# Optimization experiments

Measured on AMD Instinct MI355X. Metric: run time of the kernel, lower is better.

The kernel has to match this reference:

```python
import jax, jax.numpy as jnp
import numpy as np

B, Dx, Dz, Dy, H = 4096, 512, 512, 256, 2048
T0, T1 = 0.0, 1.0
N_STEPS = 64


def setup_inputs() -> dict:
    key = jax.random.key(0)
    ks = jax.random.split(key, 9)
    X = jax.random.normal(ks[0], (B, Dx), jnp.float32)
    # P sampled Uniform(0.01, 0.1) as in the torch module
    P = jax.random.uniform(ks[1], (Dz, Dx), jnp.float32, 0.01, 0.1)
    # A scaled so spectral radius ~1 -> exp(A*T) stays bounded over the integration
    A = jax.random.normal(ks[2], (Dz, Dz), jnp.float32) * (Dz ** -0.5)
    W1 = jax.random.normal(ks[3], (H, Dz), jnp.float32) * (Dz ** -0.5)
    b1 = jax.random.normal(ks[4], (H,), jnp.float32) * 0.01
    W2 = jax.random.normal(ks[5], (H, H), jnp.float32) * (H ** -0.5)
    b2 = jax.random.normal(ks[6], (H,), jnp.float32) * 0.01
    W3 = jax.random.normal(ks[7], (Dy, H), jnp.float32) * (H ** -0.5)
    b3 = jax.random.normal(ks[8], (Dy,), jnp.float32) * 0.01
    return dict(X=X, P=P, A=A, W1=W1, b1=b1, W2=W2, b2=b2, W3=W3, b3=b3,
                n_steps=N_STEPS)


def reference(X, P, A, W1, b1, W2, b2, W3, b3, n_steps):
    # Z0 = einsum('ji,bi->bj', P, X)  -> projection into latent ODE state
    z0 = X @ P.T  # [B, Dz]
    dt = jnp.float32((T1 - T0) / n_steps)

    def f(z):  # dz/dt = A z, batched: einsum('ji,bi->bj', A, z)
        return z @ A.T

    def rk4_step(z, _):
        k1 = f(z)
        k2 = f(z + 0.5 * dt * k1)
        k3 = f(z + 0.5 * dt * k2)
        k4 = f(z + dt * k3)
        return z + (dt / 6.0) * (k1 + 2.0 * k2 + 2.0 * k3 + k4), None

    zT, _ = jax.lax.scan(rk4_step, z0, None, length=n_steps)  # [B, Dz]

    # QnnMatrixODE MLP head (n_layers=3): Lin+ReLU, Lin+ReLU, Lin
    h = jax.nn.relu(zT @ W1.T + b1)
    h = jax.nn.relu(h @ W2.T + b2)
    y = h @ W3.T + b3  # [B, Dy]
    return y
```

## Files before the change

kernel.cpp:

```cpp
#include <hip/hip_runtime.h>

#define BDIM 4096
#define DX 512
#define DZ 512
#define DY 256
#define HD 2048
#define NSTEPS 64
#define LDT 72

typedef __attribute__((ext_vector_type(8))) short bf16x8;
typedef __attribute__((ext_vector_type(4))) float f32x4;

__device__ inline unsigned short f2bf(float f) {
    unsigned u = __float_as_uint(f);
    unsigned r = 0x7FFFu + ((u >> 16) & 1u);
    return (unsigned short)((u + r) >> 16);
}
__device__ inline float bf2f(unsigned short h) {
    return __uint_as_float(((unsigned)h) << 16);
}

#define GLDS16(g, l)                                                            \
    __builtin_amdgcn_global_load_lds((const __attribute__((address_space(1))) void*)(g), \
                                     (__attribute__((address_space(3))) void*)(l), 16, 0, 0)

struct CvtJobs {
    const float* src[5];
    unsigned short* hi[5];
    unsigned short* lo[5];
    int n4[5];
};
__global__ __launch_bounds__(256) void cvt_multi_k(CvtJobs J) {
    const int j = blockIdx.y;
    const int i4 = blockIdx.x * 256 + threadIdx.x;
    if (i4 >= J.n4[j]) return;
    float4 v = ((const float4*)J.src[j])[i4];
    ushort4 h;
    h.x = f2bf(v.x); h.y = f2bf(v.y); h.z = f2bf(v.z); h.w = f2bf(v.w);
    ((ushort4*)J.hi[j])[i4] = h;
    if (J.lo[j]) {
        ushort4 l;
        l.x = f2bf(v.x - bf2f(h.x));
        l.y = f2bf(v.y - bf2f(h.y));
        l.z = f2bf(v.z - bf2f(h.z));
        l.w = f2bf(v.w - bf2f(h.w));
        ((ushort4*)J.lo[j])[i4] = l;
    }
}

__global__ __launch_bounds__(256) void split_t_k(const float* __restrict__ A0,
                                                 unsigned short* __restrict__ H0,
                                                 unsigned short* __restrict__ L0,
                                                 const float* __restrict__ A1,
                                                 unsigned short* __restrict__ H1,
                                                 unsigned short* __restrict__ L1, int D) {
    const float* A = blockIdx.z ? A1 : A0;
    unsigned short* HT = blockIdx.z ? H1 : H0;
    unsigned short* LT = blockIdx.z ? L1 : L0;
    __shared__ float t[32][33];
    const int bx = blockIdx.x * 32, by = blockIdx.y * 32;
    const int x = threadIdx.x, y = threadIdx.y;
#pragma unroll
    for (int dy = 0; dy < 32; dy += 8)
        t[y + dy][x] = A[(size_t)(by + y + dy) * D + bx + x];
    __syncthreads();
#pragma unroll
    for (int dy = 0; dy < 32; dy += 8) {
        float v = t[x][y + dy];
        unsigned short h = f2bf(v);
        size_t o = (size_t)(bx + y + dy) * D + by + x;
        HT[o] = h;
        LT[o] = f2bf(v - bf2f(h));
    }
}

__global__ __launch_bounds__(256) void taylor_t_k(const float* __restrict__ Am,
                                                  const float* __restrict__ M2f,
                                                  const float* __restrict__ M3f,
                                                  const float* __restrict__ M4f,
                                                  unsigned short* __restrict__ Sh,
                                                  unsigned short* __restrict__ Sl,
                                                  unsigned short* __restrict__ STh,
                                                  unsigned short* __restrict__ STl,
                                                  int D, float h) {
    __shared__ float t[32][33];
    const float c2 = 0.5f * h * h;
    const float c3 = h * h * h * (1.0f / 6.0f);
    const float c4 = h * h * h * h * (1.0f / 24.0f);
    const int bx = blockIdx.x * 32, by = blockIdx.y * 32;
    const int x = threadIdx.x, y = threadIdx.y;
#pragma unroll
    for (int dy = 0; dy < 32; dy += 8) {
        const int row = by + y + dy, col = bx + x;
        const size_t idx = (size_t)row * D + col;
        float s = h * Am[idx] + c2 * M2f[idx] + c3 * M3f[idx] + c4 * M4f[idx];
        if (row == col) s += 1.0f;
        t[y + dy][x] = s;
        unsigned short hi = f2bf(s);
        Sh[idx] = hi;
        Sl[idx] = f2bf(s - bf2f(hi));
    }
    __syncthreads();
#pragma unroll
    for (int dy = 0; dy < 32; dy += 8) {
        float s = t[x][y + dy];
        size_t o = (size_t)(bx + y + dy) * D + by + x;
        unsigned short hi = f2bf(s);
        STh[o] = hi;
        STl[o] = f2bf(s - bf2f(hi));
    }
}

struct G64In { const unsigned short *Ahi, *Alo, *Bhi, *Blo; };
struct G64Out { float* Cf32; unsigned short *Chi, *Clo, *CThi, *CTlo; };

__device__ __forceinline__ void g64_core(int bx, int by, int M, int N, int K,
                                         G64In in, G64Out o,
                                         unsigned short* Ash, unsigned short* Asl,
                                         unsigned short* Bsh, unsigned short* Bsl) {
    const int tid = threadIdx.x;
    const int lane = tid & 63;
    const int wave = tid >> 6;
    const int wr = wave >> 1, wc = wave & 1;
    const int row0 = by * 64, col0 = bx * 64;
    const int sr = tid >> 2;
    const int sk = (tid & 3) * 16;

    const int niter = K >> 6;
    bf16x8 pa0, pa1, pl0, pl1, pb0, pb1, pq0, pq1;
    {
        const unsigned short* ar = in.Ahi + (size_t)(row0 + sr) * K + sk;
        const unsigned short* al = in.Alo + (size_t)(row0 + sr) * K + sk;
        const unsigned short* br = in.Bhi + (size_t)(col0 + sr) * K + sk;
        const unsigned short* bl = in.Blo + (size_t)(col0 + sr) * K + sk;
        pa0 = *(const bf16x8*)ar; pa1 = *(const bf16x8*)(ar + 8);
        pl0 = *(const bf16x8*)al; pl1 = *(const bf16x8*)(al + 8);
        pb0 = *(const bf16x8*)br; pb1 = *(const bf16x8*)(br + 8);
        pq0 = *(const bf16x8*)bl; pq1 = *(const bf16x8*)(bl + 8);
    }

    f32x4 acc[4] = {};
    const int mb = wr * 32 + (lane & 15);
    const int nb = wc * 32 + (lane & 15);

    for (int it = 0; it < niter; ++it) {
        __syncthreads();
        *(bf16x8*)&Ash[sr * LDT + sk] = pa0; *(bf16x8*)&Ash[sr * LDT + sk + 8] = pa1;
        *(bf16x8*)&Asl[sr * LDT + sk] = pl0; *(bf16x8*)&Asl[sr * LDT + sk + 8] = pl1;
        *(bf16x8*)&Bsh[sr * LDT + sk] = pb0; *(bf16x8*)&Bsh[sr * LDT + sk + 8] = pb1;
        *(bf16x8*)&Bsl[sr * LDT + sk] = pq0; *(bf16x8*)&Bsl[sr * LDT + sk + 8] = pq1;
        __syncthreads();

        {
            const int kn = (it + 1 < niter) ? ((it + 1) << 6) : 0;
            const unsigned short* ar = in.Ahi + (size_t)(row0 + sr) * K + kn + sk;
            const unsigned short* al = in.Alo + (size_t)(row0 + sr) * K + kn + sk;
            const unsigned short* br = in.Bhi + (size_t)(col0 + sr) * K + kn + sk;
            const unsigned short* bl = in.Blo + (size_t)(col0 + sr) * K + kn + sk;
            pa0 = *(const bf16x8*)ar; pa1 = *(const bf16x8*)(ar + 8);
            pl0 = *(const bf16x8*)al; pl1 = *(const bf16x8*)(al + 8);
            pb0 = *(const bf16x8*)br; pb1 = *(const bf16x8*)(br + 8);
            pq0 = *(const bf16x8*)bl; pq1 = *(const bf16x8*)(bl + 8);
        }

#pragma unroll
        for (int kh = 0; kh < 2; ++kh) {
            const int kk = kh * 32 + (lane >> 4) * 8;
            bf16x8 ah[2], alx[2], bh[2], blx[2];
#pragma unroll
            for (int t = 0; t < 2; ++t) {
                ah[t]  = *(const bf16x8*)&Ash[(mb + t * 16) * LDT + kk];
                alx[t] = *(const bf16x8*)&Asl[(mb + t * 16) * LDT + kk];
                bh[t]  = *(const bf16x8*)&Bsh[(nb + t * 16) * LDT + kk];
                blx[t] = *(const bf16x8*)&Bsl[(nb + t * 16) * LDT + kk];
            }
#pragma unroll
            for (int mt = 0; mt < 2; ++mt)
#pragma unroll
                for (int nt = 0; nt < 2; ++nt) {
                    acc[mt * 2 + nt] = __builtin_amdgcn_mfma_f32_16x16x32_bf16(
                        ah[mt], bh[nt], acc[mt * 2 + nt], 0, 0, 0);
                    acc[mt * 2 + nt] = __builtin_amdgcn_mfma_f32_16x16x32_bf16(
                        ah[mt], blx[nt], acc[mt * 2 + nt], 0, 0, 0);
                    acc[mt * 2 + nt] = __builtin_amdgcn_mfma_f32_16x16x32_bf16(
                        alx[mt], bh[nt], acc[mt * 2 + nt], 0, 0, 0);
                }
        }
    }

#pragma unroll
    for (int mt = 0; mt < 2; ++mt) {
        const int grow = row0 + wr * 32 + mt * 16 + (lane >> 4) * 4;
#pragma unroll
        for (int nt = 0; nt < 2; ++nt) {
            const int gcol = col0 + wc * 32 + nt * 16 + (lane & 15);
            f32x4 a = acc[mt * 2 + nt];
            unsigned short h4[4], l4[4];
#pragma unroll
            for (int i = 0; i < 4; ++i) {
                h4[i] = f2bf(a[i]);
                l4[i] = f2bf(a[i] - bf2f(h4[i]));
            }
            if (o.Cf32) {
#pragma unroll
                for (int i = 0; i < 4; ++i) o.Cf32[(size_t)(grow + i) * N + gcol] = a[i];
            }
            if (o.Chi) {
#pragma unroll
                for (int i = 0; i < 4; ++i) o.Chi[(size_t)(grow + i) * N + gcol] = h4[i];
            }
            if (o.Clo) {
#pragma unroll
                for (int i = 0; i < 4; ++i) o.Clo[(size_t)(grow + i) * N + gcol] = l4[i];
            }
            if (o.CThi) {
                ushort4 u = {h4[0], h4[1], h4[2], h4[3]};
                *(ushort4*)&o.CThi[(size_t)gcol * M + grow] = u;
            }
            if (o.CTlo) {
                ushort4 u = {l4[0], l4[1], l4[2], l4[3]};
                *(ushort4*)&o.CTlo[(size_t)gcol * M + grow] = u;
            }
        }
    }
}

__global__ __launch_bounds__(256) void g64_one(G64In in, G64Out o, int M, int N, int K) {
    __shared__ unsigned short Ash[64 * LDT], Asl[64 * LDT], Bsh[64 * LDT], Bsl[64 * LDT];
    g64_core(blockIdx.x, blockIdx.y, M, N, K, in, o, Ash, Asl, Bsh, Bsl);
}

__global__ __launch_bounds__(256) void g64_dual(G64In i0, G64Out o0, G64In i1, G64Out o1,
                                                int M, int N, int K) {
    __shared__ unsigned short Ash[64 * LDT], Asl[64 * LDT], Bsh[64 * LDT], Bsl[64 * LDT];
    g64_core(blockIdx.x, blockIdx.y, M, N, K, blockIdx.z ? i1 : i0, blockIdx.z ? o1 : o0,
             Ash, Asl, Bsh, Bsl);
}

template <int RELU, int BIAS, int OUT_BF16>
__global__ __launch_bounds__(256) void gemm_bf16(int M, int N, int K,
                                                 const unsigned short* __restrict__ A,
                                                 const unsigned short* __restrict__ B,
                                                 void* __restrict__ C,
                                                 const float* __restrict__ bias) {
    __shared__ unsigned short As[128 * 32];
    __shared__ unsigned short Bs[128 * 32];

    const int tid = threadIdx.x;
    const int lane = tid & 63;
    const int wave = tid >> 6;
    const int wr = wave >> 1, wc = wave & 1;
    const int row0 = blockIdx.y * 128;
    const int col0 = blockIdx.x * 128;

    const int srow = lane >> 2;
    const int schunk = (lane & 3) * 8;

    f32x4 acc[4][4] = {};

    for (int k0 = 0; k0 < K; k0 += 32) {
        const int r0 = wave * 32;
        GLDS16(A + (size_t)(row0 + r0 + srow) * K + k0 + schunk, &As[r0 * 32]);
        GLDS16(A + (size_t)(row0 + r0 + 16 + srow) * K + k0 + schunk, &As[(r0 + 16) * 32]);
        GLDS16(B + (size_t)(col0 + r0 + srow) * K + k0 + schunk, &Bs[r0 * 32]);
        GLDS16(B + (size_t)(col0 + r0 + 16 + srow) * K + k0 + schunk, &Bs[(r0 + 16) * 32]);
        __syncthreads();

        const int kk = (lane >> 4) * 8;
        const int mbase = wr * 64 + (lane & 15);
        const int nbase = wc * 64 + (lane & 15);
        bf16x8 af[4], bf[4];
#pragma unroll
        for (int t = 0; t < 4; ++t) {
            af[t] = *(const bf16x8*)&As[(mbase + t * 16) * 32 + kk];
            bf[t] = *(const bf16x8*)&Bs[(nbase + t * 16) * 32 + kk];
        }
#pragma unroll
        for (int mt = 0; mt < 4; ++mt)
#pragma unroll
            for (int nt = 0; nt < 4; ++nt)
                acc[mt][nt] = __builtin_amdgcn_mfma_f32_16x16x32_bf16(af[mt], bf[nt],
                                                                      acc[mt][nt], 0, 0, 0);
        __syncthreads();
    }

#pragma unroll
    for (int mt = 0; mt < 4; ++mt) {
        const int grow = row0 + wr * 64 + mt * 16 + (lane >> 4) * 4;
#pragma unroll
        for (int nt = 0; nt < 4; ++nt) {
            const int gcol = col0 + wc * 64 + nt * 16 + (lane & 15);
            const float bv = BIAS ? bias[gcol] : 0.0f;
#pragma unroll
            for (int i = 0; i < 4; ++i) {
                float v = acc[mt][nt][i] + bv;
                if (RELU) v = fmaxf(v, 0.0f);
                const size_t off = (size_t)(grow + i) * N + gcol;
                if (OUT_BF16)
                    ((unsigned short*)C)[off] = f2bf(v);
                else
                    ((float*)C)[off] = v;
            }
        }
    }
}

__global__ __launch_bounds__(256) void gemm64nt_f32(int M, int N, int K,
                                                    const unsigned short* __restrict__ A,
                                                    const unsigned short* __restrict__ B,
                                                    float* __restrict__ C,
                                                    const float* __restrict__ bias) {
    __shared__ unsigned short As[64 * 32];
    __shared__ unsigned short Bs[64 * 32];
    const int tid = threadIdx.x;
    const int lane = tid & 63;
    const int wave = tid >> 6;
    const int wr = wave >> 1, wc = wave & 1;
    const int row0 = blockIdx.y * 64;
    const int col0 = blockIdx.x * 64;
    const int r = tid >> 2, kq = (tid & 3) * 8;

    f32x4 acc[4] = {};

    for (int k0 = 0; k0 < K; k0 += 32) {
        bf16x8 av = *(const bf16x8*)(A + (size_t)(row0 + r) * K + k0 + kq);
        bf16x8 bv = *(const bf16x8*)(B + (size_t)(col0 + r) * K + k0 + kq);
        __syncthreads();
        *(bf16x8*)&As[r * 32 + kq] = av;
        *(bf16x8*)&Bs[r * 32 + kq] = bv;
        __syncthreads();

        const int kk = (lane >> 4) * 8;
        const int mb = wr * 32 + (lane & 15);
        const int nb = wc * 32 + (lane & 15);
        bf16x8 af[2], bf[2];
#pragma unroll
        for (int t = 0; t < 2; ++t) {
            af[t] = *(const bf16x8*)&As[(mb + t * 16) * 32 + kk];
            bf[t] = *(const bf16x8*)&Bs[(nb + t * 16) * 32 + kk];
        }
#pragma unroll
        for (int mt = 0; mt < 2; ++mt)
#pragma unroll
            for (int nt = 0; nt < 2; ++nt)
                acc[mt * 2 + nt] = __builtin_amdgcn_mfma_f32_16x16x32_bf16(
                    af[mt], bf[nt], acc[mt * 2 + nt], 0, 0, 0);
    }

#pragma unroll
    for (int mt = 0; mt < 2; ++mt) {
        const int grow = row0 + wr * 32 + mt * 16 + (lane >> 4) * 4;
#pragma unroll
        for (int nt = 0; nt < 2; ++nt) {
            const int gcol = col0 + wc * 32 + nt * 16 + (lane & 15);
            const float bv = bias ? bias[gcol] : 0.0f;
#pragma unroll
            for (int i = 0; i < 4; ++i)
                C[(size_t)(grow + i) * N + gcol] = acc[mt * 2 + nt][i] + bv;
        }
    }
}

extern "C" void kernel_launch(void* const* d_in, const int* in_sizes, int n_in,
                              void* d_out, int out_size, void* d_ws, size_t ws_size,
                              hipStream_t stream) {
    const float* X  = (const float*)d_in[0];
    const float* P  = (const float*)d_in[1];
    const float* Am = (const float*)d_in[2];
    const float* W1 = (const float*)d_in[3];
    const float* b1 = (const float*)d_in[4];
    const float* W2 = (const float*)d_in[5];
    const float* b2 = (const float*)d_in[6];
    const float* W3 = (const float*)d_in[7];
    const float* b3 = (const float*)d_in[8];
    float* out = (float*)d_out;

    const float h = 1.0f / (float)NSTEPS;
    const size_t S = (size_t)DZ * DZ;

    char* p = (char*)d_ws;
    auto alloc_f = [&](size_t n) { float* r = (float*)p; p += n * 4; return r; };
    auto alloc_h = [&](size_t n) { unsigned short* r = (unsigned short*)p; p += ((n * 2 + 15) & ~15ull); return r; };
    unsigned short* Xb   = alloc_h((size_t)BDIM * DX);
    unsigned short* W2b  = alloc_h((size_t)HD * HD);
    unsigned short* W3b  = alloc_h((size_t)DY * HD);
    unsigned short* W1h  = alloc_h((size_t)HD * DZ);
    unsigned short* W1l  = alloc_h((size_t)HD * DZ);
    unsigned short* Ah   = alloc_h(S);
    unsigned short* Al   = alloc_h(S);
    unsigned short* ATh  = alloc_h(S);
    unsigned short* ATl  = alloc_h(S);
    unsigned short* PTh  = alloc_h(S);
    unsigned short* PTl  = alloc_h(S);
    float* M2f = alloc_f(S);
    float* M3f = alloc_f(S);
    float* M4f = alloc_f(S);
    unsigned short* M2h  = alloc_h(S);
    unsigned short* M2l  = alloc_h(S);
    unsigned short* M2Th = alloc_h(S);
    unsigned short* M2Tl = alloc_h(S);
    unsigned short* Shb[2]  = {alloc_h(S), alloc_h(S)};
    unsigned short* Slb[2]  = {alloc_h(S), alloc_h(S)};
    unsigned short* SThb[2] = {alloc_h(S), alloc_h(S)};
    unsigned short* STlb[2] = {alloc_h(S), alloc_h(S)};
    unsigned short* RTh  = alloc_h(S);
    unsigned short* RTl  = alloc_h(S);
    unsigned short* C1b  = alloc_h((size_t)HD * DZ);
    unsigned short* h1b  = alloc_h((size_t)BDIM * HD);
    unsigned short* h2b  = alloc_h((size_t)BDIM * HD);

    CvtJobs J;
    J.src[0] = X;  J.hi[0] = Xb;  J.lo[0] = nullptr; J.n4[0] = BDIM * DX / 4;
    J.src[1] = W2; J.hi[1] = W2b; J.lo[1] = nullptr; J.n4[1] = HD * HD / 4;
    J.src[2] = W3; J.hi[2] = W3b; J.lo[2] = nullptr; J.n4[2] = DY * HD / 4;
    J.src[3] = W1; J.hi[3] = W1h; J.lo[3] = W1l;     J.n4[3] = HD * DZ / 4;
    J.src[4] = Am; J.hi[4] = Ah;  J.lo[4] = Al;      J.n4[4] = (int)(S / 4);
    cvt_multi_k<<<dim3(HD * HD / 4 / 256, 5), 256, 0, stream>>>(J);

    split_t_k<<<dim3(DZ / 32, DZ / 32, 2), dim3(32, 8), 0, stream>>>(
        Am, ATh, ATl, P, PTh, PTl, DZ);

    dim3 g8(DZ / 64, DZ / 64);
    const G64Out ONULL = {nullptr, nullptr, nullptr, nullptr, nullptr};

    {
        G64In i{Ah, Al, ATh, ATl};
        G64Out o{M2f, M2h, M2l, M2Th, M2Tl};
        g64_one<<<g8, 256, 0, stream>>>(i, o, DZ, DZ, DZ);
    }
    {
        G64In i0{M2h, M2l, ATh, ATl};
        G64Out o0 = ONULL; o0.Cf32 = M3f;
        G64In i1{M2h, M2l, M2Th, M2Tl};
        G64Out o1 = ONULL; o1.Cf32 = M4f;
        g64_dual<<<dim3(DZ / 64, DZ / 64, 2), 256, 0, stream>>>(i0, o0, i1, o1, DZ, DZ, DZ);
    }
    taylor_t_k<<<dim3(DZ / 32, DZ / 32), dim3(32, 8), 0, stream>>>(
        Am, M2f, M3f, M4f, Shb[0], Slb[0], SThb[0], STlb[0], DZ, h);
    int cur = 0;
    for (int s = 0; s < 6; ++s) {
        G64In i{Shb[cur], Slb[cur], SThb[cur], STlb[cur]};
        G64Out o{nullptr, Shb[1 - cur], Slb[1 - cur], SThb[1 - cur], STlb[1 - cur]};
        g64_one<<<g8, 256, 0, stream>>>(i, o, DZ, DZ, DZ);
        cur ^= 1;
    }
    {
        G64In i{Shb[cur], Slb[cur], PTh, PTl};
        G64Out o = ONULL; o.CThi = RTh; o.CTlo = RTl;
        g64_one<<<g8, 256, 0, stream>>>(i, o, DZ, DZ, DZ);
    }
    {
        G64In i{W1h, W1l, RTh, RTl};
        G64Out o = ONULL; o.Chi = C1b;
        g64_one<<<dim3(DZ / 64, HD / 64), 256, 0, stream>>>(i, o, HD, DZ, DZ);
    }

    gemm_bf16<1, 1, 1><<<dim3(HD / 128, BDIM / 128), 256, 0, stream>>>(
        BDIM, HD, DX, Xb, C1b, h1b, b1);
    gemm_bf16<1, 1, 1><<<dim3(HD / 128, BDIM / 128), 256, 0, stream>>>(
        BDIM, HD, HD, h1b, W2b, h2b, b2);
    gemm64nt_f32<<<dim3(DY / 64, BDIM / 64), 256, 0, stream>>>(
        BDIM, DY, HD, h2b, W3b, out, b3);
}
```

Baseline: 303.4 us.

## Fuse latent matrix-power chain into one persistent kernel with grid barriers

Replaces about a dozen small launches (transpose splits, Taylor series GEMMs, repeated squaring, projection and W1 composition) with a single 128-block persistent kernel that separates phases with a software grid barrier built on a global atomic counter. This removes per-launch overhead and tail gaps between tiny 512x512 GEMMs. The final output GEMM is also reworked to use 64-wide K tiles with padded LDS and register prefetch of the next tile. The grid barrier relies on all 128 blocks being co-resident, and each barrier costs atomic traffic and spinning.

```diff
diff --git a/kernel.cpp b/kernel.cpp
--- a/kernel.cpp
+++ b/kernel.cpp
@@ -7,6 +7,7 @@
 #define HD 2048
 #define NSTEPS 64
 #define LDT 72
+#define NBLK 128
 
 typedef __attribute__((ext_vector_type(8))) short bf16x8;
 typedef __attribute__((ext_vector_type(4))) float f32x4;
@@ -23,14 +24,50 @@
 #define GLDS16(g, l)                                                            \
     __builtin_amdgcn_global_load_lds((const __attribute__((address_space(1))) void*)(g), \
                                      (__attribute__((address_space(3))) void*)(l), 16, 0, 0)
+
+constexpr size_t ELS = (size_t)DZ * DZ;
+constexpr size_t OFF_BAR  = 0;
+constexpr size_t OFF_XB   = 64;
+constexpr size_t OFF_W2B  = OFF_XB   + (size_t)BDIM * DX * 2;
+constexpr size_t OFF_W3B  = OFF_W2B  + (size_t)HD * HD * 2;
+constexpr size_t OFF_W1H  = OFF_W3B  + (size_t)DY * HD * 2;
+constexpr size_t OFF_W1L  = OFF_W1H  + (size_t)HD * DZ * 2;
+constexpr size_t OFF_AH   = OFF_W1L  + (size_t)HD * DZ * 2;
+constexpr size_t OFF_AL   = OFF_AH   + ELS * 2;
+constexpr size_t OFF_ATH  = OFF_AL   + ELS * 2;
+constexpr size_t OFF_ATL  = OFF_ATH  + ELS * 2;
+constexpr size_t OFF_PTH  = OFF_ATL  + ELS * 2;
+constexpr size_t OFF_PTL  = OFF_PTH  + ELS * 2;
+constexpr size_t OFF_M2F  = OFF_PTL  + ELS * 2;
+constexpr size_t OFF_M3F  = OFF_M2F  + ELS * 4;
+constexpr size_t OFF_M4F  = OFF_M3F  + ELS * 4;
+constexpr size_t OFF_M2H  = OFF_M4F  + ELS * 4;
+constexpr size_t OFF_M2L  = OFF_M2H  + ELS * 2;
+constexpr size_t OFF_M2TH = OFF_M2L  + ELS * 2;
+constexpr size_t OFF_M2TL = OFF_M2TH + ELS * 2;
+constexpr size_t OFF_SH0  = OFF_M2TL + ELS * 2;
+constexpr size_t OFF_SL0  = OFF_SH0  + ELS * 2;
+constexpr size_t OFF_STH0 = OFF_SL0  + ELS * 2;
+constexpr size_t OFF_STL0 = OFF_STH0 + ELS * 2;
+constexpr size_t OFF_SH1  = OFF_STL0 + ELS * 2;
+constexpr size_t OFF_SL1  = OFF_SH1  + ELS * 2;
+constexpr size_t OFF_STH1 = OFF_SL1  + ELS * 2;
+constexpr size_t OFF_STL1 = OFF_STH1 + ELS * 2;
+constexpr size_t OFF_RTH  = OFF_STL1 + ELS * 2;
+constexpr size_t OFF_RTL  = OFF_RTH  + ELS * 2;
+constexpr size_t OFF_C1B  = OFF_RTL  + ELS * 2;
+constexpr size_t OFF_H1B  = OFF_C1B  + (size_t)HD * DZ * 2;
+constexpr size_t OFF_H2B  = OFF_H1B  + (size_t)BDIM * HD * 2;
 
 struct CvtJobs {
     const float* src[5];
     unsigned short* hi[5];
     unsigned short* lo[5];
     int n4[5];
+    unsigned* bar;
 };
 __global__ __launch_bounds__(256) void cvt_multi_k(CvtJobs J) {
+    if (blockIdx.x == 0 && blockIdx.y == 0 && threadIdx.x == 0) atomicExch(J.bar, 0u);
     const int j = blockIdx.y;
     const int i4 = blockIdx.x * 256 + threadIdx.x;
     if (i4 >= J.n4[j]) return;
@@ -48,67 +85,17 @@
     }
 }
 
-__global__ __launch_bounds__(256) void split_t_k(const float* __restrict__ A0,
-                                                 unsigned short* __restrict__ H0,
-                                                 unsigned short* __restrict__ L0,
-                                                 const float* __restrict__ A1,
-                                                 unsigned short* __restrict__ H1,
-                                                 unsigned short* __restrict__ L1, int D) {
-    const float* A = blockIdx.z ? A1 : A0;
-    unsigned short* HT = blockIdx.z ? H1 : H0;
-    unsigned short* LT = blockIdx.z ? L1 : L0;
-    __shared__ float t[32][33];
-    const int bx = blockIdx.x * 32, by = blockIdx.y * 32;
-    const int x = threadIdx.x, y = threadIdx.y;
-#pragma unroll
-    for (int dy = 0; dy < 32; dy += 8)
-        t[y + dy][x] = A[(size_t)(by + y + dy) * D + bx + x];
+__device__ __forceinline__ void gbar(unsigned* bar, unsigned& gen) {
+    gen += NBLK;
     __syncthreads();
-#pragma unroll
-    for (int dy = 0; dy < 32; dy += 8) {
-        float v = t[x][y + dy];
-        unsigned short h = f2bf(v);
-        size_t o = (size_t)(bx + y + dy) * D + by + x;
-        HT[o] = h;
-        LT[o] = f2bf(v - bf2f(h));
-    }
-}
-
-__global__ __launch_bounds__(256) void taylor_t_k(const float* __restrict__ Am,
-                                                  const float* __restrict__ M2f,
-                                                  const float* __restrict__ M3f,
-                                                  const float* __restrict__ M4f,
-                                                  unsigned short* __restrict__ Sh,
-                                                  unsigned short* __restrict__ Sl,
-                                                  unsigned short* __restrict__ STh,
-                                                  unsigned short* __restrict__ STl,
-                                                  int D, float h) {
-    __shared__ float t[32][33];
-    const float c2 = 0.5f * h * h;
-    const float c3 = h * h * h * (1.0f / 6.0f);
-    const float c4 = h * h * h * h * (1.0f / 24.0f);
-    const int bx = blockIdx.x * 32, by = blockIdx.y * 32;
-    const int x = threadIdx.x, y = threadIdx.y;
-#pragma unroll
-    for (int dy = 0; dy < 32; dy += 8) {
-        const int row = by + y + dy, col = bx + x;
-        const size_t idx = (size_t)row * D + col;
-        float s = h * Am[idx] + c2 * M2f[idx] + c3 * M3f[idx] + c4 * M4f[idx];
-        if (row == col) s += 1.0f;
-        t[y + dy][x] = s;
-        unsigned short hi = f2bf(s);
-        Sh[idx] = hi;
-        Sl[idx] = f2bf(s - bf2f(hi));
+    if (threadIdx.x == 0) {
+        __threadfence();
+        __hip_atomic_fetch_add(bar, 1u, __ATOMIC_RELAXED, __HIP_MEMORY_SCOPE_AGENT);
+        while (__hip_atomic_load(bar, __ATOMIC_RELAXED, __HIP_MEMORY_SCOPE_AGENT) < gen)
+            __builtin_amdgcn_s_sleep(16);
     }
     __syncthreads();
-#pragma unroll
-    for (int dy = 0; dy < 32; dy += 8) {
-        float s = t[x][y + dy];
-        size_t o = (size_t)(bx + y + dy) * D + by + x;
-        unsigned short hi = f2bf(s);
-        STh[o] = hi;
-        STl[o] = f2bf(s - bf2f(hi));
-    }
+    __threadfence();
 }
 
 struct G64In { const unsigned short *Ahi, *Alo, *Bhi, *Blo; };
@@ -225,16 +212,141 @@
     }
 }
 
-__global__ __launch_bounds__(256) void g64_one(G64In in, G64Out o, int M, int N, int K) {
-    __shared__ unsigned short Ash[64 * LDT], Asl[64 * LDT], Bsh[64 * LDT], Bsl[64 * LDT];
-    g64_core(blockIdx.x, blockIdx.y, M, N, K, in, o, Ash, Asl, Bsh, Bsl);
-}
-
-__global__ __launch_bounds__(256) void g64_dual(G64In i0, G64Out o0, G64In i1, G64Out o1,
-                                                int M, int N, int K) {
-    __shared__ unsigned short Ash[64 * LDT], Asl[64 * LDT], Bsh[64 * LDT], Bsl[64 * LDT];
-    g64_core(blockIdx.x, blockIdx.y, M, N, K, blockIdx.z ? i1 : i0, blockIdx.z ? o1 : o0,
-             Ash, Asl, Bsh, Bsl);
+__global__ __launch_bounds__(256, 1) void chain_coop(const float* __restrict__ Am,
+                                                     const float* __restrict__ P, char* ws) {
+    __shared__ __align__(16) unsigned short Ash[64 * LDT];
+    __shared__ __align__(16) unsigned short Asl[64 * LDT];
+    __shared__ __align__(16) unsigned short Bsh[64 * LDT];
+    __shared__ __align__(16) unsigned short Bsl[64 * LDT];
+
+    unsigned* bar = (unsigned*)(ws + OFF_BAR);
+    unsigned short* Ah   = (unsigned short*)(ws + OFF_AH);
+    unsigned short* Al_  = (unsigned short*)(ws + OFF_AL);
+    unsigned short* ATh  = (unsigned short*)(ws + OFF_ATH);
+    unsigned short* ATl  = (unsigned short*)(ws + OFF_ATL);
+    unsigned short* PTh  = (unsigned short*)(ws + OFF_PTH);
+    unsigned short* PTl  = (unsigned short*)(ws + OFF_PTL);
+    float* M2f = (float*)(ws + OFF_M2F);
+    float* M3f = (float*)(ws + OFF_M3F);
+    float* M4f = (float*)(ws + OFF_M4F);
+    unsigned short* M2h  = (unsigned short*)(ws + OFF_M2H);
+    unsigned short* M2l  = (unsigned short*)(ws + OFF_M2L);
+    unsigned short* M2Th = (unsigned short*)(ws + OFF_M2TH);
+    unsigned short* M2Tl = (unsigned short*)(ws + OFF_M2TL);
+    unsigned short* Shb[2]  = {(unsigned short*)(ws + OFF_SH0),  (unsigned short*)(ws + OFF_SH1)};
+    unsigned short* Slb[2]  = {(unsigned short*)(ws + OFF_SL0),  (unsigned short*)(ws + OFF_SL1)};
+    unsigned short* SThb[2] = {(unsigned short*)(ws + OFF_STH0), (unsigned short*)(ws + OFF_STH1)};
+    unsigned short* STlb[2] = {(unsigned short*)(ws + OFF_STL0), (unsigned short*)(ws + OFF_STL1)};
+    unsigned short* RTh  = (unsigned short*)(ws + OFF_RTH);
+    unsigned short* RTl  = (unsigned short*)(ws + OFF_RTL);
+    unsigned short* W1h  = (unsigned short*)(ws + OFF_W1H);
+    unsigned short* W1l  = (unsigned short*)(ws + OFF_W1L);
+    unsigned short* C1b  = (unsigned short*)(ws + OFF_C1B);
+
+    unsigned gen = 0;
+    const int blk = blockIdx.x;
+    const int x = threadIdx.x & 31, y8 = threadIdx.x >> 5;
+    float (*tls)[33] = (float(*)[33])(void*)Ash;
+
+#pragma unroll 1
+    for (int j = 0; j < 4; ++j) {
+        const int q = blk * 4 + j;
+        const float* src = (q < 256) ? Am : P;
+        unsigned short* HT = (q < 256) ? ATh : PTh;
+        unsigned short* LT = (q < 256) ? ATl : PTl;
+        const int r = q & 255;
+        const int bx = (r & 15) * 32, by = (r >> 4) * 32;
+        __syncthreads();
+#pragma unroll
+        for (int dy = 0; dy < 32; dy += 8)
+            tls[y8 + dy][x] = src[(size_t)(by + y8 + dy) * DZ + bx + x];
+        __syncthreads();
+#pragma unroll
+        for (int dy = 0; dy < 32; dy += 8) {
+            float v = tls[x][y8 + dy];
+            unsigned short h = f2bf(v);
+            size_t o = (size_t)(bx + y8 + dy) * DZ + by + x;
+            HT[o] = h;
+            LT[o] = f2bf(v - bf2f(h));
+        }
+    }
+    gbar(bar, gen);
+
+    if (blk < 64) {
+        G64In i{Ah, Al_, ATh, ATl};
+        G64Out o{M2f, M2h, M2l, M2Th, M2Tl};
+        g64_core(blk & 7, blk >> 3, DZ, DZ, DZ, i, o, Ash, Asl, Bsh, Bsl);
+    }
+    gbar(bar, gen);
+
+    {
+        G64In i = (blk < 64) ? G64In{M2h, M2l, ATh, ATl} : G64In{M2h, M2l, M2Th, M2Tl};
+        G64Out o{(blk < 64) ? M3f : M4f, nullptr, nullptr, nullptr, nullptr};
+        const int t = blk & 63;
+        g64_core(t & 7, t >> 3, DZ, DZ, DZ, i, o, Ash, Asl, Bsh, Bsl);
+    }
+    gbar(bar, gen);
+
+    {
+        const float hh = 1.0f / (float)NSTEPS;
+        const float c2 = 0.5f * hh * hh;
+        const float c3 = hh * hh * hh * (1.0f / 6.0f);
+        const float c4 = hh * hh * hh * hh * (1.0f / 24.0f);
+#pragma unroll 1
+        for (int j = 0; j < 2; ++j) {
+            const int r = blk * 2 + j;
+            const int bx = (r & 15) * 32, by = (r >> 4) * 32;
+            __syncthreads();
+#pragma unroll
+            for (int dy = 0; dy < 32; dy += 8) {
+                const int row = by + y8 + dy, col = bx + x;
+                const size_t idx = (size_t)row * DZ + col;
+                float s = hh * Am[idx] + c2 * M2f[idx] + c3 * M3f[idx] + c4 * M4f[idx];
+                if (row == col) s += 1.0f;
+                tls[y8 + dy][x] = s;
+                unsigned short hi = f2bf(s);
+                Shb[0][idx] = hi;
+                Slb[0][idx] = f2bf(s - bf2f(hi));
+            }
+            __syncthreads();
+#pragma unroll
+            for (int dy = 0; dy < 32; dy += 8) {
+                float s = tls[x][y8 + dy];
+                size_t o = (size_t)(bx + y8 + dy) * DZ + by + x;
+                unsigned short hi = f2bf(s);
+                SThb[0][o] = hi;
+                STlb[0][o] = f2bf(s - bf2f(hi));
+            }
+        }
+    }
+    gbar(bar, gen);
+
+    int cur = 0;
+#pragma unroll 1
+    for (int s = 0; s < 6; ++s) {
+        if (blk < 64) {
+            G64In i{Shb[cur], Slb[cur], SThb[cur], STlb[cur]};
+            G64Out o{nullptr, Shb[1 - cur], Slb[1 - cur], SThb[1 - cur], STlb[1 - cur]};
+            g64_core(blk & 7, blk >> 3, DZ, DZ, DZ, i, o, Ash, Asl, Bsh, Bsl);
+        }
+        gbar(bar, gen);
+        cur ^= 1;
+    }
+
+    if (blk < 64) {
+        G64In i{Shb[cur], Slb[cur], PTh, PTl};
+        G64Out o{nullptr, nullptr, nullptr, RTh, RTl};
+        g64_core(blk & 7, blk >> 3, DZ, DZ, DZ, i, o, Ash, Asl, Bsh, Bsl);
+    }
+    gbar(bar, gen);
+
+#pragma unroll 1
+    for (int j = 0; j < 2; ++j) {
+        const int t = blk + j * NBLK;
+        G64In i{W1h, W1l, RTh, RTl};
+        G64Out o{nullptr, C1b, nullptr, nullptr, nullptr};
+        g64_core(t & 7, t >> 3, HD, DZ, DZ, i, o, Ash, Asl, Bsh, Bsl);
+    }
 }
 
 template <int RELU, int BIAS, int OUT_BF16>
@@ -305,46 +417,64 @@
     }
 }
 
-__global__ __launch_bounds__(256) void gemm64nt_f32(int M, int N, int K,
-                                                    const unsigned short* __restrict__ A,
-                                                    const unsigned short* __restrict__ B,
-                                                    float* __restrict__ C,
-                                                    const float* __restrict__ bias) {
-    __shared__ unsigned short As[64 * 32];
-    __shared__ unsigned short Bs[64 * 32];
+__global__ __launch_bounds__(256) void gemm64nt_y(int M, int N, int K,
+                                                  const unsigned short* __restrict__ A,
+                                                  const unsigned short* __restrict__ B,
+                                                  float* __restrict__ C,
+                                                  const float* __restrict__ bias) {
+    __shared__ __align__(16) unsigned short As[64 * LDT];
+    __shared__ __align__(16) unsigned short Bs[64 * LDT];
     const int tid = threadIdx.x;
     const int lane = tid & 63;
     const int wave = tid >> 6;
     const int wr = wave >> 1, wc = wave & 1;
     const int row0 = blockIdx.y * 64;
     const int col0 = blockIdx.x * 64;
-    const int r = tid >> 2, kq = (tid & 3) * 8;
+    const int sr = tid >> 2, sk = (tid & 3) * 16;
+
+    const int niter = K >> 6;
+    bf16x8 pa0, pa1, pb0, pb1;
+    {
+        const unsigned short* ar = A + (size_t)(row0 + sr) * K + sk;
+        const unsigned short* br = B + (size_t)(col0 + sr) * K + sk;
+        pa0 = *(const bf16x8*)ar; pa1 = *(const bf16x8*)(ar + 8);
+        pb0 = *(const bf16x8*)br; pb1 = *(const bf16x8*)(br + 8);
+    }
 
     f32x4 acc[4] = {};
-
-    for (int k0 = 0; k0 < K; k0 += 32) {
-        bf16x8 av = *(const bf16x8*)(A + (size_t)(row0 + r) * K + k0 + kq);
-        bf16x8 bv = *(const bf16x8*)(B + (size_t)(col0 + r) * K + k0 + kq);
-        __syncthreads();
-        *(bf16x8*)&As[r * 32 + kq] = av;
-        *(bf16x8*)&Bs[r * 32 + kq] = bv;
-        __syncthreads();
-
-        const int kk = (lane >> 4) * 8;
-        const int mb = wr * 32 + (lane & 15);
-        const int nb = wc * 32 + (lane & 15);
-        bf16x8 af[2], bf[2];
-#pragma unroll
-        for (int t = 0; t < 2; ++t) {
-            af[t] = *(const bf16x8*)&As[(mb + t * 16) * 32 + kk];
-            bf[t] = *(const bf16x8*)&Bs[(nb + t * 16) * 32 + kk];
-        }
-#pragma unroll
-        for (int mt = 0; mt < 2; ++mt)
-#pragma unroll
-            for (int nt = 0; nt < 2; ++nt)
-                acc[mt * 2 + nt] = __builtin_amdgcn_mfma_f32_16x16x32_bf16(
-                    af[mt], bf[nt], acc[mt * 2 + nt], 0, 0, 0);
+    const int mb = wr * 32 + (lane & 15);
+    const int nb = wc * 32 + (lane & 15);
+
+    for (int it = 0; it < niter; ++it) {
+        __syncthreads();
+        *(bf16x8*)&As[sr * LDT + sk] = pa0; *(bf16x8*)&As[sr * LDT + sk + 8] = pa1;
+        *(bf16x8*)&Bs[sr * LDT + sk] = pb0; *(bf16x8*)&Bs[sr * LDT + sk + 8] = pb1;
+        __syncthreads();
+
+        {
+            const int kn = (it + 1 < niter) ? ((it + 1) << 6) : 0;
+            const unsigned short* ar = A + (size_t)(row0 + sr) * K + kn + sk;
+            const unsigned short* br = B + (size_t)(col0 + sr) * K + kn + sk;
+            pa0 = *(const bf16x8*)ar; pa1 = *(const bf16x8*)(ar + 8);
+            pb0 = *(const bf16x8*)br; pb1 = *(const bf16x8*)(br + 8);
+        }
+
+#pragma unroll
+        for (int kh = 0; kh < 2; ++kh) {
+            const int kk = kh * 32 + (lane >> 4) * 8;
+            bf16x8 af[2], bf[2];
+#pragma unroll
+            for (int t = 0; t < 2; ++t) {
+                af[t] = *(const bf16x8*)&As[(mb + t * 16) * LDT + kk];
+                bf[t] = *(const bf16x8*)&Bs[(nb + t * 16) * LDT + kk];
+            }
+#pragma unroll
+            for (int mt = 0; mt < 2; ++mt)
+#pragma unroll
+                for (int nt = 0; nt < 2; ++nt)
+                    acc[mt * 2 + nt] = __builtin_amdgcn_mfma_f32_16x16x32_bf16(
+                        af[mt], bf[nt], acc[mt * 2 + nt], 0, 0, 0);
+        }
     }
 
 #pragma unroll
@@ -375,90 +505,33 @@
     const float* b3 = (const float*)d_in[8];
     float* out = (float*)d_out;
 
-    const float h = 1.0f / (float)NSTEPS;
-    const size_t S = (size_t)DZ * DZ;
-
-    char* p = (char*)d_ws;
-    auto alloc_f = [&](size_t n) { float* r = (float*)p; p += n * 4; return r; };
-    auto alloc_h = [&](size_t n) { unsigned short* r = (unsigned short*)p; p += ((n * 2 + 15) & ~15ull); return r; };
-    unsigned short* Xb   = alloc_h((size_t)BDIM * DX);
-    unsigned short* W2b  = alloc_h((size_t)HD * HD);
-    unsigned short* W3b  = alloc_h((size_t)DY * HD);
-    unsigned short* W1h  = alloc_h((size_t)HD * DZ);
-    unsigned short* W1l  = alloc_h((size_t)HD * DZ);
-    unsigned short* Ah   = alloc_h(S);
-    unsigned short* Al   = alloc_h(S);
-    unsigned short* ATh  = alloc_h(S);
-    unsigned short* ATl  = alloc_h(S);
-    unsigned short* PTh  = alloc_h(S);
-    unsigned short* PTl  = alloc_h(S);
-    float* M2f = alloc_f(S);
-    float* M3f = alloc_f(S);
-    float* M4f = alloc_f(S);
-    unsigned short* M2h  = alloc_h(S);
-    unsigned short* M2l  = alloc_h(S);
-    unsigned short* M2Th = alloc_h(S);
-    unsigned short* M2Tl = alloc_h(S);
-    unsigned short* Shb[2]  = {alloc_h(S), alloc_h(S)};
-    unsigned short* Slb[2]  = {alloc_h(S), alloc_h(S)};
-    unsigned short* SThb[2] = {alloc_h(S), alloc_h(S)};
-    unsigned short* STlb[2] = {alloc_h(S), alloc_h(S)};
-    unsigned short* RTh  = alloc_h(S);
-    unsigned short* RTl  = alloc_h(S);
-    unsigned short* C1b  = alloc_h((size_t)HD * DZ);
-    unsigned short* h1b  = alloc_h((size_t)BDIM * HD);
-    unsigned short* h2b  = alloc_h((size_t)BDIM * HD);
+    char* ws = (char*)d_ws;
+    unsigned short* Xb  = (unsigned short*)(ws + OFF_XB);
+    unsigned short* W2b = (unsigned short*)(ws + OFF_W2B);
+    unsigned short* W3b = (unsigned short*)(ws + OFF_W3B);
+    unsigned short* W1h = (unsigned short*)(ws + OFF_W1H);
+    unsigned short* W1l = (unsigned short*)(ws + OFF_W1L);
+    unsigned short* Ah  = (unsigned short*)(ws + OFF_AH);
+    unsigned short* Al  = (unsigned short*)(ws + OFF_AL);
+    unsigned short* C1b = (unsigned short*)(ws + OFF_C1B);
+    unsigned short* h1b = (unsigned short*)(ws + OFF_H1B);
+    unsigned short* h2b = (unsigned short*)(ws + OFF_H2B);
 
     CvtJobs J;
     J.src[0] = X;  J.hi[0] = Xb;  J.lo[0] = nullptr; J.n4[0] = BDIM * DX / 4;
     J.src[1] = W2; J.hi[1] = W2b; J.lo[1] = nullptr; J.n4[1] = HD * HD / 4;
     J.src[2] = W3; J.hi[2] = W3b; J.lo[2] = nullptr; J.n4[2] = DY * HD / 4;
     J.src[3] = W1; J.hi[3] = W1h; J.lo[3] = W1l;     J.n4[3] = HD * DZ / 4;
-    J.src[4] = Am; J.hi[4] = Ah;  J.lo[4] = Al;      J.n4[4] = (int)(S / 4);
+    J.src[4] = Am; J.hi[4] = Ah;  J.lo[4] = Al;      J.n4[4] = (int)(ELS / 4);
+    J.bar = (unsigned*)(ws + OFF_BAR);
     cvt_multi_k<<<dim3(HD * HD / 4 / 256, 5), 256, 0, stream>>>(J);
 
-    split_t_k<<<dim3(DZ / 32, DZ / 32, 2), dim3(32, 8), 0, stream>>>(
-        Am, ATh, ATl, P, PTh, PTl, DZ);
-
-    dim3 g8(DZ / 64, DZ / 64);
-    const G64Out ONULL = {nullptr, nullptr, nullptr, nullptr, nullptr};
-
-    {
-        G64In i{Ah, Al, ATh, ATl};
-        G64Out o{M2f, M2h, M2l, M2Th, M2Tl};
-        g64_one<<<g8, 256, 0, stream>>>(i, o, DZ, DZ, DZ);
-    }
-    {
-        G64In i0{M2h, M2l, ATh, ATl};
-        G64Out o0 = ONULL; o0.Cf32 = M3f;
-        G64In i1{M2h, M2l, M2Th, M2Tl};
-        G64Out o1 = ONULL; o1.Cf32 = M4f;
-        g64_dual<<<dim3(DZ / 64, DZ / 64, 2), 256, 0, stream>>>(i0, o0, i1, o1, DZ, DZ, DZ);
-    }
-    taylor_t_k<<<dim3(DZ / 32, DZ / 32), dim3(32, 8), 0, stream>>>(
-        Am, M2f, M3f, M4f, Shb[0], Slb[0], SThb[0], STlb[0], DZ, h);
-    int cur = 0;
-    for (int s = 0; s < 6; ++s) {
-        G64In i{Shb[cur], Slb[cur], SThb[cur], STlb[cur]};
-        G64Out o{nullptr, Shb[1 - cur], Slb[1 - cur], SThb[1 - cur], STlb[1 - cur]};
-        g64_one<<<g8, 256, 0, stream>>>(i, o, DZ, DZ, DZ);
-        cur ^= 1;
-    }
-    {
-        G64In i{Shb[cur], Slb[cur], PTh, PTl};
-        G64Out o = ONULL; o.CThi = RTh; o.CTlo = RTl;
-        g64_one<<<g8, 256, 0, stream>>>(i, o, DZ, DZ, DZ);
-    }
-    {
-        G64In i{W1h, W1l, RTh, RTl};
-        G64Out o = ONULL; o.Chi = C1b;
-        g64_one<<<dim3(DZ / 64, HD / 64), 256, 0, stream>>>(i, o, HD, DZ, DZ);
-    }
+    chain_coop<<<dim3(NBLK), 256, 0, stream>>>(Am, P, ws);
 
     gemm_bf16<1, 1, 1><<<dim3(HD / 128, BDIM / 128), 256, 0, stream>>>(
         BDIM, HD, DX, Xb, C1b, h1b, b1);
     gemm_bf16<1, 1, 1><<<dim3(HD / 128, BDIM / 128), 256, 0, stream>>>(
         BDIM, HD, HD, h1b, W2b, h2b, b2);
-    gemm64nt_f32<<<dim3(DY / 64, BDIM / 64), 256, 0, stream>>>(
+    gemm64nt_y<<<dim3(DY / 64, BDIM / 64), 256, 0, stream>>>(
         BDIM, DY, HD, h2b, W3b, out, b3);
 }
```

Measured after the change: 473.3 us. +56.0%, slower.
